# Optimization experiments

Measured on AMD Instinct MI355X. Metric: run time of the kernel, lower is better.

Reference implementation:

```python
import jax, jax.numpy as jnp
import numpy as np

# ---- layer config (yolov3, layer_no=2) ----
STRIDE = 8
N_CLASSES = 80
IGNORE_TH = 0.7
ANCHORS_PX = np.array([[10,13],[16,30],[33,23],[30,61],[62,45],[59,119],[116,90],[156,198],[373,326]], np.float32)
ALL_ANCHORS = ANCHORS_PX / STRIDE          # [9,2] in grid units
ANCHOR_ID_LO, ANCHOR_ID_HI = 0, 2          # anchor_mask[2] = [0,1,2]
ANCHORS = ALL_ANCHORS[ANCHOR_ID_LO:ANCHOR_ID_HI+1]  # [3,2]
NA = 3
NC = N_CLASSES + 5

B, IN_CH, NG, NBOX = 16, 256, 76, 50


def _safe_log(p):
    # emulate torch BCE's log clamp at -100; eps stops 0*inf -> nan
    return jnp.maximum(jnp.log(jnp.maximum(p, 1e-12)), -100.0)


def _bce_sum(p, t, w=None):
    l = -(t * _safe_log(p) + (1.0 - t) * _safe_log(1.0 - p))
    if w is not None:
        l = l * w
    return l.sum()


def setup_inputs() -> dict:
    key = jax.random.key(0)
    k1, k2, k3, k4, k5 = jax.random.split(key, 5)
    xin = jax.random.normal(k1, (B, IN_CH, NG, NG), jnp.float32)
    cls = jax.random.randint(k2, (B, NBOX, 1), 0, N_CLASSES).astype(jnp.float32)
    cxy = jax.random.uniform(k3, (B, NBOX, 2), jnp.float32, 0.02, 0.98)
    wh = jax.random.uniform(k4, (B, NBOX, 2), jnp.float32, 0.02, 0.40)
    labels = jnp.concatenate([cls, cxy, wh], axis=-1)  # [B,N,5]
    W = jax.random.normal(k5, (NA * NC, IN_CH), jnp.float32) * 0.02  # 1x1 conv
    b = jnp.zeros((NA * NC,), jnp.float32)
    return {"xin": xin, "labels": labels, "W": W, "b": b}


def _yolo_loss(xin, labels, W, b):
    nB, _, nG, _ = xin.shape
    anchors = jnp.asarray(ANCHORS, xin.dtype)          # [3,2]
    all_anchors = jnp.asarray(ALL_ANCHORS, xin.dtype)  # [9,2]

    # 1x1 conv -> [B, A, G, G, C]
    x = jnp.einsum('bchw,oc->bohw', xin, W) + b[None, :, None, None]
    x = x.reshape(nB, NA, NC, nG, nG).transpose(0, 1, 3, 4, 2)

    xy = jax.nn.sigmoid(x[..., :2])
    wh = x[..., 2:4]
    conf_cls = jax.nn.sigmoid(x[..., 4:])  # [B,A,G,G,1+ncls]

    gy, gx = jnp.meshgrid(jnp.arange(nG, dtype=x.dtype), jnp.arange(nG, dtype=x.dtype), indexing='ij')
    pred_boxes = jnp.stack([
        xy[..., 0] + gx,
        xy[..., 1] + gy,
        jnp.exp(wh[..., 0]) * anchors[:, 0][None, :, None, None],
        jnp.exp(wh[..., 1]) * anchors[:, 1][None, :, None, None]], axis=-1)  # [B,A,G,G,4]

    # ---- ground truth ----
    valid = labels.sum(-1) > 0                     # [B,N]
    gt_cls = labels[..., 0].astype(jnp.int32)
    gt = labels[..., 1:] * nG                      # [B,N,4] cx,cy,w,h in grid units
    gt_x, gt_y, gt_w, gt_h = gt[..., 0], gt[..., 1], gt[..., 2], gt[..., 3]
    gi = jnp.floor(gt_x).astype(jnp.int32)
    gj = jnp.floor(gt_y).astype(jnp.int32)

    # best anchor per gt: wh-IoU vs all 9 anchors (centered at origin)
    inter_a = jnp.minimum(gt_w[..., None], all_anchors[:, 0]) * jnp.minimum(gt_h[..., None], all_anchors[:, 1])
    union_a = gt_w[..., None] * gt_h[..., None] + all_anchors[:, 0] * all_anchors[:, 1] - inter_a
    best = jnp.argmax(inter_a / union_a, axis=-1)  # [B,N]
    in_mask = (best >= ANCHOR_ID_LO) & (best <= ANCHOR_ID_HI)
    a = jnp.where(in_mask, best % 3, -1)           # [B,N]

    # all-pairs IoU: pred boxes vs gt boxes (ignore mask)
    pb = pred_boxes.reshape(nB, -1, 4)             # [B,M,4], M = A*G*G
    pa_area = pb[..., 2] * pb[..., 3]
    gt_area = gt_w * gt_h
    tl = jnp.maximum(pb[:, :, None, :2] - pb[:, :, None, 2:] / 2, gt[:, None, :, :2] - gt[:, None, :, 2:] / 2)
    br = jnp.minimum(pb[:, :, None, :2] + pb[:, :, None, 2:] / 2, gt[:, None, :, :2] + gt[:, None, :, 2:] / 2)
    inter = jnp.prod(br - tl, -1) * jnp.all(tl < br, -1)
    iou = inter / (pa_area[:, :, None] + gt_area[:, None, :] - inter)
    iou = jnp.where(valid[:, None, :], iou, 0.0)
    best_iou = iou.max(-1)                         # [B,M]
    has_boxes = valid.any(-1)
    obj_mask = jnp.where(has_boxes[:, None], best_iou <= IGNORE_TH, True).reshape(nB, NA, nG, nG)

    # ---- scatter target assignment ----
    assign = valid & (a >= 0)
    a_safe = jnp.clip(a, 0, NA - 1)
    aw = anchors[a_safe, 0]
    ah = anchors[a_safe, 1]
    tvec = jnp.concatenate([
        (gt_x - jnp.floor(gt_x))[..., None],
        (gt_y - jnp.floor(gt_y))[..., None],
        jnp.log(gt_w / aw + 1e-16)[..., None],
        jnp.log(gt_h / ah + 1e-16)[..., None],
        jnp.ones_like(gt_x)[..., None],
        jax.nn.one_hot(gt_cls, N_CLASSES, dtype=x.dtype)], axis=-1)  # [B,N,NC]
    sval = 2.0 - gt_w * gt_h / (nG * nG)

    bf = jnp.broadcast_to(jnp.arange(nB)[:, None], a.shape).reshape(-1)
    af = jnp.where(assign, a_safe, NA).reshape(-1)  # NA is OOB -> dropped
    jf = gj.reshape(-1)
    if_ = gi.reshape(-1)

    target = jnp.zeros((nB, NA, nG, nG, NC), x.dtype).at[bf, af, jf, if_].set(tvec.reshape(-1, NC), mode='drop')
    scale = jnp.zeros((nB, NA, nG, nG), x.dtype).at[bf, af, jf, if_].set(sval.reshape(-1), mode='drop')
    obj_mask = obj_mask.at[bf, af, jf, if_].set(True, mode='drop')
    noobj = jnp.zeros((nB, NA, nG, nG), bool).at[bf, af, jf, if_].set(True, mode='drop')

    # ---- losses ----
    nm = noobj.astype(x.dtype)[..., None]
    p_obj = conf_cls[..., 0] * obj_mask
    t_obj = target[..., 4] * obj_mask
    p_xy = xy * nm
    t_xy = target[..., :2] * nm
    p_wh = wh * nm
    t_wh = target[..., 2:4] * nm
    p_cls = conf_cls[..., 1:] * nm
    t_cls = target[..., 5:] * nm
    sc = scale[..., None]

    loss_xy = _bce_sum(p_xy, t_xy, sc)
    rs = jnp.sqrt(sc)
    loss_wh = 0.5 * jnp.sum((p_wh * rs - t_wh * rs) ** 2)
    loss_obj = _bce_sum(p_obj, t_obj)
    loss_cls = _bce_sum(p_cls, t_cls)
    loss = loss_xy + loss_wh + loss_obj + loss_cls
    return jnp.stack([loss, loss_xy, loss_wh, loss_obj, loss_cls])


def reference(xin, labels, W, b):
    return _yolo_loss(xin, labels, W, b)
```

## Files before the change

kernel.cpp:

```cpp
#include <hip/hip_runtime.h>
#include <math.h>

#define NB    16
#define NAg   3
#define NCg   85
#define NCLS  80
#define NGg   76
#define NSp   (NGg*NGg)
#define NBOX  50
#define INCH  256
#define SPB   256
#define GBLK  ((NSp + SPB - 1) / SPB)
#define TOTBLK (GBLK * NB)

#define ACC_OFF  0
#define HAS_OFF  32
#define DONE_OFF 96
#define WT_OFF   128
#define GB_OFF   (WT_OFF + 16384)
#define GA_OFF   (GB_OFF + 25600)
#define GI_OFF   (GA_OFF + 25600)

__device__ __constant__ float c_AW[9] = {1.25f,2.0f,4.125f,3.75f,7.75f,7.375f,14.5f,19.5f,46.625f};
__device__ __constant__ float c_AH[9] = {1.625f,3.75f,2.875f,7.625f,5.625f,14.875f,11.25f,24.75f,40.75f};

__device__ __forceinline__ float safe_log(float p) {
    return fmaxf(logf(fmaxf(p, 1e-12f)), -100.0f);
}
__device__ __forceinline__ float sigm(float x) {
    return 1.0f / (1.0f + expf(-x));
}

__global__ __launch_bounds__(256) void k_labels(
    const float* __restrict__ labels, const float* __restrict__ W,
    float* __restrict__ Wt, float* __restrict__ gbox, float* __restrict__ gaux,
    int* __restrict__ gint, int* __restrict__ hasAny, float* __restrict__ acc,
    int* __restrict__ done)
{
    const int b = blockIdx.x, tid = threadIdx.x;
    const int t = b * 256 + tid;

    {
        const int c = t >> 4, f = t & 15;
        Wt[t] = (f < 15) ? W[((f / 5) * NCg + (f % 5)) * INCH + c] : 0.f;
    }
    if (b == 0 && tid < 8)  acc[tid] = 0.f;
    if (b == 0 && tid == 8) *done = 0;

    int valid = 0;
    if (tid < NBOX) {
        const int bt = b * NBOX + tid;
        const float* L = labels + (size_t)bt * 5;
        const float l0 = L[0], l1 = L[1], l2 = L[2], l3 = L[3], l4 = L[4];
        valid = (l0 + l1 + l2 + l3 + l4) > 0.f;

        const float gx = l1 * NGg, gy = l2 * NGg, gw = l3 * NGg, gh = l4 * NGg;

        int best = 0; float brr = -1.f;
#pragma unroll
        for (int k = 0; k < 9; k++) {
            float inter = fminf(gw, c_AW[k]) * fminf(gh, c_AH[k]);
            float uni   = gw*gh + c_AW[k]*c_AH[k] - inter;
            float r     = inter / uni;
            if (r > brr) { brr = r; best = k; }
        }
        const int a = (best <= 2) ? best : -1;
        const int assign = valid && (a >= 0);
        const int a_safe = a < 0 ? 0 : (a > 2 ? 2 : a);

        const int gi = (int)floorf(gx), gj = (int)floorf(gy);
        const int inb = (gi >= 0) && (gi < NGg) && (gj >= 0) && (gj < NGg);
        const int cell = (assign && inb) ? (a * NSp + gj * NGg + gi) : -1;

        float* gb = gbox + (size_t)bt * 8;
        gb[0] = gx - gw * 0.5f;
        gb[1] = gy - gh * 0.5f;
        gb[2] = gx + gw * 0.5f;
        gb[3] = gy + gh * 0.5f;
        gb[4] = valid ? gw * gh : -1.f;
        gb[5] = __int_as_float(cell);

        float* ga = gaux + (size_t)bt * 8;
        ga[0] = gx - floorf(gx);
        ga[1] = gy - floorf(gy);
        ga[2] = logf(gw / c_AW[a_safe] + 1e-16f);
        ga[3] = logf(gh / c_AH[a_safe] + 1e-16f);
        ga[4] = 2.f - gw * gh / (float)NSp;

        gint[bt*2 + 0] = cell;
        gint[bt*2 + 1] = (int)l0;
    }
    if (tid < 64) {
        const unsigned long long m = __ballot(valid != 0);
        if (tid == 0) hasAny[b] = (m != 0ULL) ? 1 : 0;
    }
}

__global__ __launch_bounds__(256) void k_main(
    const float* __restrict__ xin, const float* __restrict__ Wt,
    const float* __restrict__ W, const float* __restrict__ bias,
    const float* __restrict__ gbox, const float* __restrict__ gaux,
    const int* __restrict__ gint, const int* __restrict__ hasAny,
    float* __restrict__ acc, int* __restrict__ done, float* __restrict__ out)
{
    __shared__ float part[4][15][SPB];
    __shared__ float wred[4];

    const int bx  = blockIdx.x;
    const int b   = blockIdx.y;
    const int tid = threadIdx.x;
    const int w   = tid >> 6, l = tid & 63;
    const int wu  = __builtin_amdgcn_readfirstlane(w);
    const int pb  = bx * SPB;

    float4 ac[15];
#pragma unroll
    for (int f = 0; f < 15; ++f) ac[f] = make_float4(0.f,0.f,0.f,0.f);

    const float* xp = xin + ((size_t)b * INCH + (wu << 6)) * NSp + pb + 4*l;
    const float* wp = Wt + ((wu << 6) << 4);

    if (pb + SPB <= NSp) {
        for (int c0 = 0; c0 < 64; c0 += 8) {
            float4 v[8];
#pragma unroll
            for (int k = 0; k < 8; ++k)
                v[k] = *(const float4*)(xp + (size_t)(c0 + k) * NSp);
#pragma unroll
            for (int k = 0; k < 8; ++k) {
                const float* wr = wp + ((c0 + k) << 4);
#pragma unroll
                for (int f = 0; f < 15; ++f) {
                    const float wv = wr[f];
                    ac[f].x += wv * v[k].x;  ac[f].y += wv * v[k].y;
                    ac[f].z += wv * v[k].z;  ac[f].w += wv * v[k].w;
                }
            }
        }
    } else {
        const bool lv = (pb + 4*l) < NSp;
        const float4 z = make_float4(0.f,0.f,0.f,0.f);
        for (int c0 = 0; c0 < 64; c0 += 8) {
            float4 v[8];
#pragma unroll
            for (int k = 0; k < 8; ++k)
                v[k] = lv ? *(const float4*)(xp + (size_t)(c0 + k) * NSp) : z;
#pragma unroll
            for (int k = 0; k < 8; ++k) {
                const float* wr = wp + ((c0 + k) << 4);
#pragma unroll
                for (int f = 0; f < 15; ++f) {
                    const float wv = wr[f];
                    ac[f].x += wv * v[k].x;  ac[f].y += wv * v[k].y;
                    ac[f].z += wv * v[k].z;  ac[f].w += wv * v[k].w;
                }
            }
        }
    }

#pragma unroll
    for (int f = 0; f < 15; ++f)
        *(float4*)&part[w][f][4*l] = ac[f];
    __syncthreads();

    float lsum = 0.f;
    const int p = pb + tid;
    if (p < NSp) {
        float xv[15];
#pragma unroll
        for (int f = 0; f < 15; ++f)
            xv[f] = part[0][f][tid] + part[1][f][tid]
                  + part[2][f][tid] + part[3][f][tid];

        const int sy = p / NGg;
        const int sx = p - sy * NGg;
        const float gxf = (float)sx, gyf = (float)sy;

        float pbx0[3], pby0[3], pbx1[3], pby1[3], pa[3], cf[3];
#pragma unroll
        for (int a = 0; a < 3; ++a) {
            const float px = sigm(xv[a*5+0] + bias[a*NCg+0]) + gxf;
            const float py = sigm(xv[a*5+1] + bias[a*NCg+1]) + gyf;
            const float pw = expf(xv[a*5+2] + bias[a*NCg+2]) * c_AW[a];
            const float ph = expf(xv[a*5+3] + bias[a*NCg+3]) * c_AH[a];
            cf[a]   = sigm(xv[a*5+4] + bias[a*NCg+4]);
            pbx0[a] = px - pw * 0.5f;  pby0[a] = py - ph * 0.5f;
            pbx1[a] = px + pw * 0.5f;  pby1[a] = py + ph * 0.5f;
            pa[a]   = pw * ph;
        }

        int mask = 0;
        const float* gb = gbox + (size_t)b * NBOX * 8;
        for (int n = 0; n < NBOX; ++n) {
            const float bx0 = gb[n*8+0], by0 = gb[n*8+1];
            const float bx1 = gb[n*8+2], by1 = gb[n*8+3];
            const float gar = gb[n*8+4];
            const int cell  = __float_as_int(gb[n*8+5]);
            const int d = cell - p;
            if (d == 0)       mask |= 8;
            if (d == NSp)     mask |= 16;
            if (d == 2*NSp)   mask |= 32;
            if (gar >= 0.f) {
#pragma unroll
                for (int a = 0; a < 3; ++a) {
                    const float tlx = fmaxf(pbx0[a], bx0);
                    const float tly = fmaxf(pby0[a], by0);
                    const float brx = fminf(pbx1[a], bx1);
                    const float bry = fminf(pby1[a], by1);
                    const float dx = brx - tlx, dy = bry - tly;
                    const float inter = (dx > 0.f && dy > 0.f) ? dx * dy : 0.f;
                    if (inter > 0.7f * (pa[a] + gar - inter)) mask |= (1 << a);
                }
            }
        }

        const bool hasB = hasAny[b] != 0;
#pragma unroll
        for (int a = 0; a < 3; ++a) {
            const bool ex = (mask & (1 << a)) != 0;
            const bool as = (mask & (8 << a)) != 0;
            const bool maskpre = hasB ? (!ex) : true;
            if (maskpre || as) {
                const float c = cf[a];
                lsum += as ? -safe_log(c) : -safe_log(1.f - c);
            }
        }
    }

#pragma unroll
    for (int off = 32; off > 0; off >>= 1) lsum += __shfl_down(lsum, off);
    if (l == 0) wred[w] = lsum;
    __syncthreads();
    if (tid == 0) atomicAdd(&acc[2], wred[0] + wred[1] + wred[2] + wred[3]);

    int*   scell = (int*)&part[0][0][0];
    float* colv  = &part[0][1][0];
    float* xsh   = &part[0][2][0];
    float* sacc  = &part[0][3][0];

    if (tid < NBOX) scell[tid] = gint[(b * NBOX + tid) * 2];
    __syncthreads();

    for (int n = bx; n < NBOX; n += GBLK) {
        const int cell = scell[n];
        bool win = (cell >= 0);
        if (win)
            for (int n2 = n + 1; n2 < NBOX; ++n2)
                if (scell[n2] == cell) { win = false; break; }

        if (win) {
            const int a = cell / NSp, s = cell % NSp;
            const int o0 = a * NCg;
            const int t  = b * NBOX + n;

            colv[tid] = xin[((size_t)b * INCH + tid) * NSp + s];
            if (tid < 3) sacc[tid] = 0.f;
            __syncthreads();

            for (int o = w; o < NCg; o += 4) {
                const float4 wv = *(const float4*)&W[(size_t)(o0 + o) * INCH + l * 4];
                const float4 cv = *(const float4*)&colv[l * 4];
                float pr = wv.x*cv.x + wv.y*cv.y + wv.z*cv.z + wv.w*cv.w;
                for (int off = 32; off; off >>= 1) pr += __shfl_down(pr, off);
                if (l == 0) xsh[o] = pr + bias[o0 + o];
            }
            __syncthreads();

            if (tid < NCg) {
                const float* ga = gaux + (size_t)t * 8;
                const float sval = ga[4];
                const int gcls = gint[t*2 + 1];
                float val = xsh[tid];
                float term; int slot;
                if (tid < 2) {
                    float tgt = ga[tid];
                    float pp = sigm(val);
                    term = -(tgt * safe_log(pp) + (1.f - tgt) * safe_log(1.f - pp)) * sval;
                    slot = 0;
                } else if (tid < 4) {
                    float tgt = ga[tid];
                    float d = val - tgt;
                    term = 0.5f * sval * d * d;
                    slot = 1;
                } else if (tid == 4) {
                    term = 0.f; slot = 2;
                } else {
                    float tgt = ((tid - 5) == gcls) ? 1.f : 0.f;
                    float pp = sigm(val);
                    term = -(tgt * safe_log(pp) + (1.f - tgt) * safe_log(1.f - pp));
                    slot = 2;
                }
                atomicAdd(&sacc[slot], term);
            }
            __syncthreads();
            if (tid == 0) {
                atomicAdd(&acc[0], sacc[0]);
                atomicAdd(&acc[1], sacc[1]);
                atomicAdd(&acc[3], sacc[2]);
            }
            __syncthreads();
        }
    }

    if (tid == 0) {
        __threadfence();
        const int v = atomicAdd(done, 1);
        if (v == TOTBLK - 1) {
            const float xy = atomicAdd(&acc[0], 0.f);
            const float wh = atomicAdd(&acc[1], 0.f);
            const float ob = atomicAdd(&acc[2], 0.f);
            const float cl = atomicAdd(&acc[3], 0.f);
            out[0] = xy + wh + ob + cl;
            out[1] = xy; out[2] = wh; out[3] = ob; out[4] = cl;
        }
    }
}

extern "C" void kernel_launch(void* const* d_in, const int* in_sizes, int n_in,
                              void* d_out, int out_size, void* d_ws, size_t ws_size,
                              hipStream_t stream)
{
    const float* xin    = (const float*)d_in[0];
    const float* labels = (const float*)d_in[1];
    const float* W      = (const float*)d_in[2];
    const float* bias   = (const float*)d_in[3];

    char* ws = (char*)d_ws;
    float* acc    = (float*)(ws + ACC_OFF);
    int*   hasAny = (int*)  (ws + HAS_OFF);
    int*   done   = (int*)  (ws + DONE_OFF);
    float* Wt     = (float*)(ws + WT_OFF);
    float* gbox   = (float*)(ws + GB_OFF);
    float* gaux   = (float*)(ws + GA_OFF);
    int*   gint   = (int*)  (ws + GI_OFF);
    float* out    = (float*)d_out;

    k_labels<<<16, 256, 0, stream>>>(labels, W, Wt, gbox, gaux, gint, hasAny, acc, done);

    k_main<<<dim3(GBLK, NB), 256, 0, stream>>>(xin, Wt, W, bias, gbox, gaux,
                                               gint, hasAny, acc, done, out);
}
```

Baseline: 196.6 us.

## Double-buffer channel loads in conv loop and prefetch GT columns early

The full-tile 1x1 conv loop is rewritten as a manually unrolled double-buffered schedule, so the next 8 channel float4 loads are in flight while FMAs run on the previous group. The ground-truth box winner check and the gather of that cell's input column now happen at kernel start, so those scattered global loads overlap with the main compute. This raises register pressure (two 8-float4 buffers plus 60 accumulators and prefetched values), which could lower occupancy or cause spills.

```diff
diff --git a/kernel.cpp b/kernel.cpp
--- a/kernel.cpp
+++ b/kernel.cpp
@@ -96,6 +96,18 @@
     }
 }
 
+#define LOADG(buf, c0base) \
+    { _Pragma("unroll") for (int k = 0; k < 8; ++k) \
+        buf[k] = *(const float4*)(xp + (size_t)((c0base) + k) * NSp); }
+
+#define FMAG(buf, c0base) \
+    { _Pragma("unroll") for (int k = 0; k < 8; ++k) { \
+        const float* wr = wp + (((c0base) + k) << 4); \
+        _Pragma("unroll") for (int f = 0; f < 15; ++f) { \
+            const float wv = wr[f]; \
+            ac[f].x += wv * buf[k].x;  ac[f].y += wv * buf[k].y; \
+            ac[f].z += wv * buf[k].z;  ac[f].w += wv * buf[k].w; } } }
+
 __global__ __launch_bounds__(256) void k_main(
     const float* __restrict__ xin, const float* __restrict__ Wt,
     const float* __restrict__ W, const float* __restrict__ bias,
@@ -105,6 +117,7 @@
 {
     __shared__ float part[4][15][SPB];
     __shared__ float wred[4];
+    __shared__ int   scell[NBOX];
 
     const int bx  = blockIdx.x;
     const int b   = blockIdx.y;
@@ -113,6 +126,26 @@
     const int wu  = __builtin_amdgcn_readfirstlane(w);
     const int pb  = bx * SPB;
 
+    if (tid < NBOX) scell[tid] = gint[(b * NBOX + tid) * 2];
+    __syncthreads();
+
+    int  tcell[3]; bool twin[3]; float tcol[3];
+#pragma unroll
+    for (int i = 0; i < 3; ++i) {
+        const int n = bx + i * GBLK;
+        tcell[i] = (n < NBOX) ? scell[n] : -1;
+        bool wn = tcell[i] >= 0;
+        if (wn)
+            for (int n2 = n + 1; n2 < NBOX; ++n2)
+                if (scell[n2] == tcell[i]) { wn = false; break; }
+        twin[i] = wn;
+        tcol[i] = 0.f;
+        if (wn) {
+            const int s = tcell[i] % NSp;
+            tcol[i] = xin[((size_t)b * INCH + tid) * NSp + s];
+        }
+    }
+
     float4 ac[15];
 #pragma unroll
     for (int f = 0; f < 15; ++f) ac[f] = make_float4(0.f,0.f,0.f,0.f);
@@ -121,22 +154,23 @@
     const float* wp = Wt + ((wu << 6) << 4);
 
     if (pb + SPB <= NSp) {
-        for (int c0 = 0; c0 < 64; c0 += 8) {
-            float4 v[8];
-#pragma unroll
-            for (int k = 0; k < 8; ++k)
-                v[k] = *(const float4*)(xp + (size_t)(c0 + k) * NSp);
-#pragma unroll
-            for (int k = 0; k < 8; ++k) {
-                const float* wr = wp + ((c0 + k) << 4);
-#pragma unroll
-                for (int f = 0; f < 15; ++f) {
-                    const float wv = wr[f];
-                    ac[f].x += wv * v[k].x;  ac[f].y += wv * v[k].y;
-                    ac[f].z += wv * v[k].z;  ac[f].w += wv * v[k].w;
-                }
-            }
-        }
+        float4 va[8], vb[8];
+        LOADG(va, 0)
+        LOADG(vb, 8)
+        FMAG (va, 0)
+        LOADG(va, 16)
+        FMAG (vb, 8)
+        LOADG(vb, 24)
+        FMAG (va, 16)
+        LOADG(va, 32)
+        FMAG (vb, 24)
+        LOADG(vb, 40)
+        FMAG (va, 32)
+        LOADG(va, 48)
+        FMAG (vb, 40)
+        LOADG(vb, 56)
+        FMAG (va, 48)
+        FMAG (vb, 56)
     } else {
         const bool lv = (pb + 4*l) < NSp;
         const float4 z = make_float4(0.f,0.f,0.f,0.f);
@@ -233,27 +267,20 @@
     __syncthreads();
     if (tid == 0) atomicAdd(&acc[2], wred[0] + wred[1] + wred[2] + wred[3]);
 
-    int*   scell = (int*)&part[0][0][0];
     float* colv  = &part[0][1][0];
     float* xsh   = &part[0][2][0];
     float* sacc  = &part[0][3][0];
 
-    if (tid < NBOX) scell[tid] = gint[(b * NBOX + tid) * 2];
-    __syncthreads();
-
-    for (int n = bx; n < NBOX; n += GBLK) {
-        const int cell = scell[n];
-        bool win = (cell >= 0);
-        if (win)
-            for (int n2 = n + 1; n2 < NBOX; ++n2)
-                if (scell[n2] == cell) { win = false; break; }
-
-        if (win) {
-            const int a = cell / NSp, s = cell % NSp;
+#pragma unroll
+    for (int i = 0; i < 3; ++i) {
+        if (twin[i]) {
+            const int n    = bx + i * GBLK;
+            const int cell = tcell[i];
+            const int a = cell / NSp;
             const int o0 = a * NCg;
             const int t  = b * NBOX + n;
 
-            colv[tid] = xin[((size_t)b * INCH + tid) * NSp + s];
+            colv[tid] = tcol[i];
             if (tid < 3) sacc[tid] = 0.f;
             __syncthreads();
 
```

Result: no change. 195.0 us (-0.8%).

## Halve spatial tile and assign matched boxes to owning block

Applied to the files above, without the earlier changes.

The spatial tile per block drops from 256 to 128 pixels, with each lane loading float2 instead of float4, which doubles the grid and lowers register use. Each block now handles only the ground-truth boxes whose cell falls inside its own tile. It captures those input columns from the main conv loads into shared memory instead of re-reading xin. It also reuses the already reduced box and conf channels, so only the 80 class rows need a separate dot product. The trade-offs are half of each block's threads idling during the per-pixel loss, a serial winner scan on thread 0, and a fallback path when more than four boxes land in one tile.

```diff
diff --git a/kernel.cpp b/kernel.cpp
--- a/kernel.cpp
+++ b/kernel.cpp
@@ -9,9 +9,12 @@
 #define NSp   (NGg*NGg)
 #define NBOX  50
 #define INCH  256
-#define SPB   256
+#define NG2   (NSp/2)
+#define SPB   128
+#define GPB   64
 #define GBLK  ((NSp + SPB - 1) / SPB)
 #define TOTBLK (GBLK * NB)
+#define NWCAP 4
 
 #define ACC_OFF  0
 #define HAS_OFF  32
@@ -96,15 +99,22 @@
     }
 }
 
-__global__ __launch_bounds__(256) void k_main(
+__global__ __launch_bounds__(256) void k_mega(
     const float* __restrict__ xin, const float* __restrict__ Wt,
     const float* __restrict__ W, const float* __restrict__ bias,
     const float* __restrict__ gbox, const float* __restrict__ gaux,
     const int* __restrict__ gint, const int* __restrict__ hasAny,
     float* __restrict__ acc, int* __restrict__ done, float* __restrict__ out)
 {
-    __shared__ float part[4][15][SPB];
-    __shared__ float wred[4];
+    __shared__ float2 buf[4][15][GPB];
+    __shared__ __align__(16) float cls_col[NWCAP][256];
+    __shared__ int   scell[NBOX];
+    __shared__ int   winf[NBOX];
+    __shared__ int   wlN[NBOX], wlS[NBOX];
+    __shared__ int   nwinS;
+    __shared__ float xsh[NCg];
+    __shared__ float sacc[3];
+    __shared__ float wred[2];
 
     const int bx  = blockIdx.x;
     const int b   = blockIdx.y;
@@ -113,64 +123,88 @@
     const int wu  = __builtin_amdgcn_readfirstlane(w);
     const int pb  = bx * SPB;
 
-    float4 ac[15];
-#pragma unroll
-    for (int f = 0; f < 15; ++f) ac[f] = make_float4(0.f,0.f,0.f,0.f);
-
-    const float* xp = xin + ((size_t)b * INCH + (wu << 6)) * NSp + pb + 4*l;
-    const float* wp = Wt + ((wu << 6) << 4);
-
-    if (pb + SPB <= NSp) {
+    if (tid < NBOX) scell[tid] = gint[(b * NBOX + tid) * 2];
+    __syncthreads();
+    if (tid < NBOX) {
+        const int cell = scell[tid];
+        int f = (cell >= 0);
+        for (int n2 = tid + 1; n2 < NBOX; ++n2)
+            if (scell[n2] == cell) { f = 0; break; }
+        winf[tid] = f;
+    }
+    __syncthreads();
+    if (tid == 0) {
+        int c = 0;
+        for (int n = 0; n < NBOX; ++n) {
+            if (winf[n]) {
+                const int sw = scell[n] % NSp;
+                if (sw >= pb && sw < pb + SPB) { wlN[c] = n; wlS[c] = sw; ++c; }
+            }
+        }
+        nwinS = c;
+    }
+    __syncthreads();
+
+    const int nwin = nwinS;
+    int lwj[NWCAP], eej[NWCAP];
+#pragma unroll
+    for (int j = 0; j < NWCAP; ++j) {
+        const int sw = (j < nwin) ? wlS[j] : pb;
+        lwj[j] = (sw - pb) >> 1;
+        eej[j] = sw & 1;
+    }
+
+    const int G   = bx * GPB + l;
+    const bool liveG = (G < NG2);
+
+    float2 a2[15];
+#pragma unroll
+    for (int f = 0; f < 15; ++f) a2[f] = make_float2(0.f, 0.f);
+
+    if (liveG) {
+        const float* xp = xin + ((size_t)b * INCH + (wu << 6)) * NSp + (G << 1);
+        const float* wp = Wt + ((wu << 6) << 4);
+#pragma unroll 2
         for (int c0 = 0; c0 < 64; c0 += 8) {
-            float4 v[8];
+            float2 v[8];
 #pragma unroll
             for (int k = 0; k < 8; ++k)
-                v[k] = *(const float4*)(xp + (size_t)(c0 + k) * NSp);
+                v[k] = *(const float2*)(xp + (size_t)(c0 + k) * NSp);
 #pragma unroll
             for (int k = 0; k < 8; ++k) {
                 const float* wr = wp + ((c0 + k) << 4);
 #pragma unroll
                 for (int f = 0; f < 15; ++f) {
-                    const float wv = wr[f];
-                    ac[f].x += wv * v[k].x;  ac[f].y += wv * v[k].y;
-                    ac[f].z += wv * v[k].z;  ac[f].w += wv * v[k].w;
+                    a2[f].x += wr[f] * v[k].x;
+                    a2[f].y += wr[f] * v[k].y;
                 }
             }
-        }
-    } else {
-        const bool lv = (pb + 4*l) < NSp;
-        const float4 z = make_float4(0.f,0.f,0.f,0.f);
-        for (int c0 = 0; c0 < 64; c0 += 8) {
-            float4 v[8];
-#pragma unroll
-            for (int k = 0; k < 8; ++k)
-                v[k] = lv ? *(const float4*)(xp + (size_t)(c0 + k) * NSp) : z;
-#pragma unroll
-            for (int k = 0; k < 8; ++k) {
-                const float* wr = wp + ((c0 + k) << 4);
-#pragma unroll
-                for (int f = 0; f < 15; ++f) {
-                    const float wv = wr[f];
-                    ac[f].x += wv * v[k].x;  ac[f].y += wv * v[k].y;
-                    ac[f].z += wv * v[k].z;  ac[f].w += wv * v[k].w;
+#pragma unroll
+            for (int j = 0; j < NWCAP; ++j) {
+                if (j < nwin && l == lwj[j]) {
+#pragma unroll
+                    for (int k = 0; k < 8; ++k)
+                        cls_col[j][(wu << 6) + c0 + k] = eej[j] ? v[k].y : v[k].x;
                 }
             }
         }
     }
-
-#pragma unroll
-    for (int f = 0; f < 15; ++f)
-        *(float4*)&part[w][f][4*l] = ac[f];
+#pragma unroll
+    for (int f = 0; f < 15; ++f) buf[w][f][l] = a2[f];
     __syncthreads();
 
     float lsum = 0.f;
     const int p = pb + tid;
-    if (p < NSp) {
+    if (tid < SPB && p < NSp) {
+        const int g = tid >> 1, e = tid & 1;
         float xv[15];
 #pragma unroll
-        for (int f = 0; f < 15; ++f)
-            xv[f] = part[0][f][tid] + part[1][f][tid]
-                  + part[2][f][tid] + part[3][f][tid];
+        for (int f = 0; f < 15; ++f) {
+            xv[f] = ((const float*)&buf[0][f][g])[e]
+                  + ((const float*)&buf[1][f][g])[e]
+                  + ((const float*)&buf[2][f][g])[e]
+                  + ((const float*)&buf[3][f][g])[e];
+        }
 
         const int sy = p / NGg;
         const int sx = p - sy * NGg;
@@ -229,76 +263,78 @@
 
 #pragma unroll
     for (int off = 32; off > 0; off >>= 1) lsum += __shfl_down(lsum, off);
-    if (l == 0) wred[w] = lsum;
-    __syncthreads();
-    if (tid == 0) atomicAdd(&acc[2], wred[0] + wred[1] + wred[2] + wred[3]);
-
-    int*   scell = (int*)&part[0][0][0];
-    float* colv  = &part[0][1][0];
-    float* xsh   = &part[0][2][0];
-    float* sacc  = &part[0][3][0];
-
-    if (tid < NBOX) scell[tid] = gint[(b * NBOX + tid) * 2];
-    __syncthreads();
-
-    for (int n = bx; n < NBOX; n += GBLK) {
+    if (w < 2 && l == 0) wred[w] = lsum;
+    __syncthreads();
+    if (tid == 0) atomicAdd(&acc[2], wred[0] + wred[1]);
+
+    for (int j = 0; j < nwin; ++j) {
+        __syncthreads();
+        const int n    = wlN[j];
         const int cell = scell[n];
-        bool win = (cell >= 0);
-        if (win)
-            for (int n2 = n + 1; n2 < NBOX; ++n2)
-                if (scell[n2] == cell) { win = false; break; }
-
-        if (win) {
-            const int a = cell / NSp, s = cell % NSp;
-            const int o0 = a * NCg;
-            const int t  = b * NBOX + n;
-
-            colv[tid] = xin[((size_t)b * INCH + tid) * NSp + s];
-            if (tid < 3) sacc[tid] = 0.f;
+        const int a    = cell / NSp;
+        const int sw   = cell % NSp;
+        const int o0   = a * NCg;
+        const int t    = b * NBOX + n;
+        const int pp   = sw - pb;
+        const int g    = pp >> 1, e = pp & 1;
+
+        if (j >= NWCAP) {
+            cls_col[0][tid] = xin[((size_t)b * INCH + tid) * NSp + sw];
             __syncthreads();
-
-            for (int o = w; o < NCg; o += 4) {
-                const float4 wv = *(const float4*)&W[(size_t)(o0 + o) * INCH + l * 4];
-                const float4 cv = *(const float4*)&colv[l * 4];
-                float pr = wv.x*cv.x + wv.y*cv.y + wv.z*cv.z + wv.w*cv.w;
-                for (int off = 32; off; off >>= 1) pr += __shfl_down(pr, off);
-                if (l == 0) xsh[o] = pr + bias[o0 + o];
-            }
-            __syncthreads();
-
-            if (tid < NCg) {
-                const float* ga = gaux + (size_t)t * 8;
-                const float sval = ga[4];
-                const int gcls = gint[t*2 + 1];
-                float val = xsh[tid];
-                float term; int slot;
-                if (tid < 2) {
-                    float tgt = ga[tid];
-                    float pp = sigm(val);
-                    term = -(tgt * safe_log(pp) + (1.f - tgt) * safe_log(1.f - pp)) * sval;
-                    slot = 0;
-                } else if (tid < 4) {
-                    float tgt = ga[tid];
-                    float d = val - tgt;
-                    term = 0.5f * sval * d * d;
-                    slot = 1;
-                } else if (tid == 4) {
-                    term = 0.f; slot = 2;
-                } else {
-                    float tgt = ((tid - 5) == gcls) ? 1.f : 0.f;
-                    float pp = sigm(val);
-                    term = -(tgt * safe_log(pp) + (1.f - tgt) * safe_log(1.f - pp));
-                    slot = 2;
-                }
-                atomicAdd(&sacc[slot], term);
-            }
-            __syncthreads();
-            if (tid == 0) {
-                atomicAdd(&acc[0], sacc[0]);
-                atomicAdd(&acc[1], sacc[1]);
-                atomicAdd(&acc[3], sacc[2]);
-            }
-            __syncthreads();
+        }
+        const float* col = cls_col[j < NWCAP ? j : 0];
+
+        for (int o2 = w; o2 < NCLS; o2 += 4) {
+            const int row = o0 + 5 + o2;
+            const float4 wv = *(const float4*)&W[(size_t)row * INCH + l * 4];
+            const float4 cv = *(const float4*)&col[l * 4];
+            float pr = wv.x*cv.x + wv.y*cv.y + wv.z*cv.z + wv.w*cv.w;
+            for (int off = 32; off; off >>= 1) pr += __shfl_down(pr, off);
+            if (l == 0) xsh[5 + o2] = pr + bias[row];
+        }
+        if (tid < 4) {
+            const int f = a * 5 + tid;
+            const float raw = ((const float*)&buf[0][f][g])[e]
+                            + ((const float*)&buf[1][f][g])[e]
+                            + ((const float*)&buf[2][f][g])[e]
+                            + ((const float*)&buf[3][f][g])[e];
+            xsh[tid] = raw + bias[a*NCg + tid];
+        }
+        if (tid == 4) xsh[4] = 0.f;
+        if (tid < 3) sacc[tid] = 0.f;
+        __syncthreads();
+
+        if (tid < NCg) {
+            const float* ga = gaux + (size_t)t * 8;
+            const float sval = ga[4];
+            const int gcls = gint[t*2 + 1];
+            float val = xsh[tid];
+            float term; int slot;
+            if (tid < 2) {
+                float tgt = ga[tid];
+                float pp2 = sigm(val);
+                term = -(tgt * safe_log(pp2) + (1.f - tgt) * safe_log(1.f - pp2)) * sval;
+                slot = 0;
+            } else if (tid < 4) {
+                float tgt = ga[tid];
+                float d = val - tgt;
+                term = 0.5f * sval * d * d;
+                slot = 1;
+            } else if (tid == 4) {
+                term = 0.f; slot = 2;
+            } else {
+                float tgt = ((tid - 5) == gcls) ? 1.f : 0.f;
+                float pp2 = sigm(val);
+                term = -(tgt * safe_log(pp2) + (1.f - tgt) * safe_log(1.f - pp2));
+                slot = 2;
+            }
+            atomicAdd(&sacc[slot], term);
+        }
+        __syncthreads();
+        if (tid == 0) {
+            atomicAdd(&acc[0], sacc[0]);
+            atomicAdd(&acc[1], sacc[1]);
+            atomicAdd(&acc[3], sacc[2]);
         }
     }
 
@@ -337,6 +373,6 @@
 
     k_labels<<<16, 256, 0, stream>>>(labels, W, Wt, gbox, gaux, gint, hasAny, acc, done);
 
-    k_main<<<dim3(GBLK, NB), 256, 0, stream>>>(xin, Wt, W, bias, gbox, gaux,
+    k_mega<<<dim3(GBLK, NB), 256, 0, stream>>>(xin, Wt, W, bias, gbox, gaux,
                                                gint, hasAny, acc, done, out);
 }
```

Result: slower. 203.8 us (+3.7%).
